# Performance work log

Measured on AMD Instinct MI355X. Metric: run time of the kernel, lower is better.

Reference implementation:

```python
import jax, jax.numpy as jnp
import numpy as np

NUM_HEADS = 4
IN_CHANNELS = 256
SCALE = IN_CHANNELS ** (-0.5)  # scaled=True uses in_channels, not hidden


def setup_inputs() -> dict:
    key = jax.random.key(0)
    ks = jax.random.split(key, 6)
    B, C, H, W = 8, 256, 48, 48
    hid = 128
    std_e = (2.0 / (3 * hid)) ** 0.5   # kaiming fan_out for 1x1 conv
    std_o = (2.0 / C) ** 0.5
    return {
        "x0": jax.random.normal(ks[0], (B, C, H, W), jnp.float32),
        "x1": jax.random.normal(ks[1], (B, C, H, W), jnp.float32),
        "embed_w0": jax.random.normal(ks[2], (3 * hid, C), jnp.float32) * std_e,
        "embed_b0": jnp.zeros((3 * hid,), jnp.float32),
        "embed_w1": jax.random.normal(ks[3], (3 * hid, C), jnp.float32) * std_e,
        "embed_b1": jnp.zeros((3 * hid,), jnp.float32),
        "out_w0": jax.random.normal(ks[4], (hid * NUM_HEADS, C), jnp.float32) * std_o,
        "out_b0": jnp.zeros((C,), jnp.float32),
        "out_w1": jax.random.normal(ks[5], (hid * NUM_HEADS, C), jnp.float32) * std_o,
        "out_b1": jnp.zeros((C,), jnp.float32),
    }


def _embed(x, w, b):
    # 1x1 conv: [B,C,H,W] x [3h,C] -> [B,3h,H,W], then flatten spatial and split q/k/v
    e = jnp.einsum('bchw,oc->bohw', x, w) + b[None, :, None, None]
    B, O, H, W = e.shape
    e = e.reshape(B, O, H * W)
    return jnp.split(e, 3, axis=1)  # each [B, h, N]


def _attend(q, k, v):
    # q from the OTHER stream; softmax over keys (last dim)
    attn = jax.nn.softmax(jnp.einsum('bcm,bcn->bmn', q, k) * SCALE, axis=-1)
    return jnp.einsum('bmn,bcn->bcm', attn, v)  # [B, h, N]


def _output(h, x, w, b):
    # all NUM_HEADS heads are identical (same embed conv reused per head),
    # so the concat along channels is a tile of one head.
    hh = jnp.tile(h, (1, NUM_HEADS, 1))  # [B, h*nh, N]
    # 1x1 transposed conv == pointwise linear with weight [h*nh, C]
    o = jnp.einsum('bcm,co->bom', hh, w) + b[None, :, None]
    return o.reshape(x.shape) + x  # residual


def reference(x0, x1, embed_w0, embed_b0, embed_w1, embed_b1,
              out_w0, out_b0, out_w1, out_b1):
    q0, k0, v0 = _embed(x0, embed_w0, embed_b0)
    q1, k1, v1 = _embed(x1, embed_w1, embed_b1)
    h0 = _attend(q1, k0, v0)  # stream 0 queried by stream 1's q
    h1 = _attend(q0, k1, v1)
    out0 = _output(h0, x0, out_w0, out_b0)
    out1 = _output(h1, x1, out_w1, out_b1)
    return (out0, out1)
```

## Files before the change

kernel.cpp:

```cpp
#include <hip/hip_runtime.h>
#include <stdint.h>

#define B_   8
#define C_   256
#define N_   2304
#define HID  128
#define O3   384
#define NH   4
#define SCALE 0.0625f
#define QPRE 0.09016844f

typedef unsigned short u16;
typedef short  bf8  __attribute__((ext_vector_type(8)));
typedef float  f4   __attribute__((ext_vector_type(4)));
typedef u16    u16x8 __attribute__((ext_vector_type(8)));

#define MFMA(a,b,c) __builtin_amdgcn_mfma_f32_16x16x32_bf16((a),(b),(c),0,0,0)

static __device__ __forceinline__ u16 f2bf(float f){
    union { float f; unsigned int i; } v; v.f = f;
    unsigned int r = v.i + 0x7FFFu + ((v.i >> 16) & 1u);
    return (u16)(r >> 16);
}
static __device__ __forceinline__ float fexp2(float x){
#if __has_builtin(__builtin_amdgcn_exp2f)
    return __builtin_amdgcn_exp2f(x);
#else
    return __expf(x * 0.69314718f);
#endif
}
static __device__ __forceinline__ u16 hi16(float f){
    union { float f; unsigned int i; } v; v.f = f;
    return (u16)(v.i >> 16);
}
static __device__ __forceinline__ void dma16(const void* g, void* l){
    __builtin_amdgcn_global_load_lds(
        (const __attribute__((address_space(1))) void*)g,
        (__attribute__((address_space(3))) void*)l, 16, 0, 0);
}

__global__ __launch_bounds__(256) void k_prep(const float* __restrict__ ew0,
                                              const float* __restrict__ ew1,
                                              const float* __restrict__ ow0,
                                              const float* __restrict__ ow1,
                                              u16* __restrict__ Wbf,
                                              u16* __restrict__ weff){
    int bid = blockIdx.x;
    if (bid < 192){
        int s = bid >= 96 ? 1 : 0;
        int xb = bid - s*96;
        const float* w = s ? ew1 : ew0;
        u16* o = Wbf + (size_t)s * (O3 * C_);
        int idx = (xb * 256 + threadIdx.x) * 4;
        float4 v = *reinterpret_cast<const float4*>(&w[idx]);
        o[idx+0] = f2bf(v.x); o[idx+1] = f2bf(v.y);
        o[idx+2] = f2bf(v.z); o[idx+3] = f2bf(v.w);
    } else {
        int gid = (bid - 192) * 256 + threadIdx.x;
        int oc = gid & 255, hc = (gid >> 8) & 127, s = gid >> 15;
        const float* w = s ? ow1 : ow0;
        float acc = 0.f;
        #pragma unroll
        for (int h = 0; h < NH; ++h) acc += w[(h*HID + hc)*C_ + oc];
        weff[(s*C_ + oc)*HID + hc] = f2bf(acc);
    }
}

__global__ __launch_bounds__(256, 3) void k_embed_fused(
        const float* __restrict__ x0, const float* __restrict__ x1,
        const u16* __restrict__ Wbf,
        const float* __restrict__ b0, const float* __restrict__ b1,
        u16* __restrict__ Qc, u16* __restrict__ Kc, u16* __restrict__ Vc){
    __shared__ __align__(16) u16 Xs[64*272];
    __shared__ __align__(16) u16 tile[64*72];
    int z = blockIdx.y, bb = z >> 1, s = z & 1;
    const float* X = (s ? x1 : x0) + (size_t)bb * (C_ * N_);
    const u16* W = Wbf + (size_t)s * (O3 * C_);
    const float* bias = s ? b1 : b0;
    int n0 = blockIdx.x * 64;
    int t = threadIdx.x;
    int lane = t & 63, wave = t >> 6;
    int l16 = lane & 15, quad = lane >> 4;

    {
        int lr = t >> 4, lc = (t & 15) * 4;
        int row = t >> 3, col8 = (t & 7) * 8;
        for (int cb = 0; cb < 4; ++cb){
            int c0 = cb * 64;
            #pragma unroll
            for (int rep = 0; rep < 4; ++rep){
                int c = lr + rep * 16;
                float4 v = *reinterpret_cast<const float4*>(
                    &X[(size_t)(c0 + c) * N_ + n0 + lc]);
                tile[c*65 + lc+0] = f2bf(v.x); tile[c*65 + lc+1] = f2bf(v.y);
                tile[c*65 + lc+2] = f2bf(v.z); tile[c*65 + lc+3] = f2bf(v.w);
            }
            __syncthreads();
            #pragma unroll
            for (int rep = 0; rep < 2; ++rep){
                int n = row + rep * 32;
                u16x8 v;
                #pragma unroll
                for (int j = 0; j < 8; ++j) v[j] = tile[(col8 + j)*65 + n];
                *reinterpret_cast<u16x8*>(&Xs[n*272 + c0 + col8]) = v;
            }
            __syncthreads();
        }
    }

    size_t zq = (size_t)z * (N_ * HID);
    int ncw = n0 >> 6;
    for (int og = 0; og < 6; ++og){
        int o0 = og*64 + wave*16;
        f4 acc[4] = {f4{0,0,0,0}, f4{0,0,0,0}, f4{0,0,0,0}, f4{0,0,0,0}};
        #pragma unroll
        for (int kk = 0; kk < 8; ++kk){
            bf8 a = *reinterpret_cast<const bf8*>(&W[(o0 + l16)*C_ + kk*32 + quad*8]);
            #pragma unroll
            for (int nt = 0; nt < 4; ++nt){
                bf8 bv = *reinterpret_cast<const bf8*>(
                    &Xs[(nt*16 + l16)*272 + kk*32 + quad*8]);
                acc[nt] = MFMA(a, bv, acc[nt]);
            }
        }
        float4 bv4 = *reinterpret_cast<const float4*>(&bias[o0 + quad*4]);
        float bb4[4] = {bv4.x, bv4.y, bv4.z, bv4.w};
        #pragma unroll
        for (int nt = 0; nt < 4; ++nt)
            #pragma unroll
            for (int r = 0; r < 4; ++r){
                float e = acc[nt][r] + bb4[r];
                if (og < 2) e *= QPRE;
                tile[(wave*16 + quad*4 + r)*72 + nt*16 + l16] = f2bf(e);
            }
        __syncthreads();
        #pragma unroll
        for (int rep = 0; rep < 2; ++rep){
            int idx = t + rep*256;
            if (og < 2){
                int n = idx & 63, g8 = idx >> 6;
                u16x8 v;
                #pragma unroll
                for (int j = 0; j < 8; ++j) v[j] = tile[(g8*8 + j)*72 + n];
                int ng = n0 + n;
                *reinterpret_cast<u16x8*>(&Qc[zq + (size_t)(ng>>4)*2048
                        + (og*8 + g8)*128 + (ng & 15)*8]) = v;
            } else if (og < 4){
                int n = idx & 63, cc = idx >> 6;
                u16x8 v;
                #pragma unroll
                for (int j = 0; j < 8; ++j) v[j] = tile[(cc*8 + j)*72 + n];
                *reinterpret_cast<u16x8*>(&Kc[zq
                        + (size_t)(ncw*16 + (og-2)*8 + cc)*512 + n*8]) = v;
            } else {
                int hl = idx & 63, p = idx >> 6;
                u16x8 v = *reinterpret_cast<const u16x8*>(&tile[hl*72 + p*8]);
                *reinterpret_cast<u16x8*>(&Vc[zq + (size_t)(ncw*8 + p)*1024
                        + ((og-4)*64 + hl)*8]) = v;
            }
        }
        __syncthreads();
    }
}

__global__ __launch_bounds__(256, 3) void k_attn_out(const u16* __restrict__ Qt,
        const u16* __restrict__ Kc, const u16* __restrict__ Vc,
        const u16* __restrict__ weff,
        const float* __restrict__ ob0, const float* __restrict__ ob1,
        const float* __restrict__ x0, const float* __restrict__ x1,
        float* __restrict__ out){
    __shared__ __align__(16) u16 kbuf[64*128];
    __shared__ __align__(16) u16 vbuf[64*128];
    __shared__ __align__(16) u16 smem[8*16*72];
    int bx = blockIdx.x;
    int xcd = bx & 7, t = bx >> 3;
    int z  = xcd*2 + (t >= 36 ? 1 : 0);
    int mt = (t >= 36) ? (t - 36) : t;
    int b = z >> 1, s = z & 1;
    const u16* Q = Qt + (size_t)(b*2 + (1 - s)) * (N_ * HID);
    const u16* K = Kc + (size_t)(b*2 + s)       * (N_ * HID);
    const u16* V = Vc + (size_t)(b*2 + s)       * (N_ * HID);
    const u16* Wf   = weff + (size_t)s * (C_ * HID);
    const float* bias = s ? ob1 : ob0;
    const float* X = (s ? x1 : x0) + (size_t)b * (C_ * N_);
    float* O = out + (size_t)s * ((size_t)B_ * C_ * N_) + (size_t)b * (C_ * N_);
    int lane = threadIdx.x & 63, wave = threadIdx.x >> 6;
    int l16 = lane & 15, quad = lane >> 4;
    int m0 = mt * 64 + wave * 16;

    bf8 aq[4];
    {
        const u16* Qb = Q + (size_t)(m0 >> 4)*2048 + l16*8;
        #pragma unroll
        for (int kk = 0; kk < 4; ++kk)
            aq[kk] = *reinterpret_cast<const bf8*>(&Qb[(kk*4 + quad)*128]);
    }

    bf8 ones;
    #pragma unroll
    for (int j = 0; j < 8; ++j) ones[j] = (short)0x3F80;

    f4 oacc[8];
    #pragma unroll
    for (int ct = 0; ct < 8; ++ct) oacc[ct] = f4{0,0,0,0};
    f4 sumacc = f4{0,0,0,0};

    const char* Kb = (const char*)K;
    const char* Vb = (const char*)V;

    for (int nc = 0; nc < N_/64; ++nc){
        __syncthreads();
        #pragma unroll
        for (int j = 0; j < 4; ++j){
            int ik = wave*4 + j;
            dma16(Kb + ((size_t)(nc*16 + ik)*512 + lane*8)*2, &kbuf[ik*512]);
        }
        #pragma unroll
        for (int j = 0; j < 4; ++j){
            int iv = wave*4 + j;
            dma16(Vb + ((size_t)(nc*8 + (iv>>1))*1024 + (iv&1)*512 + lane*8)*2,
                  &vbuf[iv*512]);
        }
        __syncthreads();
        f4 sacc[4] = {f4{0,0,0,0}, f4{0,0,0,0}, f4{0,0,0,0}, f4{0,0,0,0}};
        #pragma unroll
        for (int kk = 0; kk < 4; ++kk)
            #pragma unroll
            for (int nt = 0; nt < 4; ++nt){
                bf8 bk = *reinterpret_cast<const bf8*>(&kbuf[((kk*4+quad)*64 + nt*16 + l16)*8]);
                sacc[nt] = MFMA(aq[kk], bk, sacc[nt]);
            }
        u16* pw = smem + (wave*2 + (nc & 1)) * (16*72);
        #pragma unroll
        for (int nt = 0; nt < 4; ++nt)
            #pragma unroll
            for (int r = 0; r < 4; ++r)
                pw[(quad*4 + r)*72 + nt*16 + l16] = hi16(fexp2(sacc[nt][r]));
        #pragma unroll
        for (int kk2 = 0; kk2 < 2; ++kk2){
            bf8 ap = *reinterpret_cast<const bf8*>(&pw[l16*72 + kk2*32 + quad*8]);
            sumacc = MFMA(ap, ones, sumacc);
            #pragma unroll
            for (int ct = 0; ct < 8; ++ct){
                bf8 bv = *reinterpret_cast<const bf8*>(&vbuf[((kk2*4+quad)*128 + ct*16 + l16)*8]);
                oacc[ct] = MFMA(ap, bv, oacc[ct]);
            }
        }
    }

    __syncthreads();
    float inv[4];
    #pragma unroll
    for (int r = 0; r < 4; ++r) inv[r] = 1.0f / sumacc[r];
    #pragma unroll
    for (int ct = 0; ct < 8; ++ct)
        #pragma unroll
        for (int r = 0; r < 4; ++r)
            smem[(wave*16 + quad*4 + r)*136 + ct*16 + l16] = f2bf(oacc[ct][r] * inv[r]);
    __syncthreads();

    int mb = mt * 64;
    int oc0 = wave * 64;
    f4 acc2[4][4];
    #pragma unroll
    for (int ot = 0; ot < 4; ++ot)
        #pragma unroll
        for (int nt = 0; nt < 4; ++nt) acc2[ot][nt] = f4{0,0,0,0};
    #pragma unroll
    for (int kk = 0; kk < 4; ++kk){
        bf8 bh[4];
        #pragma unroll
        for (int nt = 0; nt < 4; ++nt)
            bh[nt] = *reinterpret_cast<const bf8*>(&smem[(nt*16 + l16)*136 + kk*32 + quad*8]);
        #pragma unroll
        for (int ot = 0; ot < 4; ++ot){
            bf8 a = *reinterpret_cast<const bf8*>(&Wf[(oc0 + ot*16 + l16)*HID + kk*32 + quad*8]);
            #pragma unroll
            for (int nt = 0; nt < 4; ++nt)
                acc2[ot][nt] = MFMA(a, bh[nt], acc2[ot][nt]);
        }
    }
    #pragma unroll
    for (int ot = 0; ot < 4; ++ot)
        #pragma unroll
        for (int nt = 0; nt < 4; ++nt){
            int m = mb + nt*16 + l16;
            #pragma unroll
            for (int r = 0; r < 4; ++r){
                int oc = oc0 + ot*16 + quad*4 + r;
                O[(size_t)oc*N_ + m] = acc2[ot][nt][r] + bias[oc] + X[(size_t)oc*N_ + m];
            }
        }
}

extern "C" void kernel_launch(void* const* d_in, const int* in_sizes, int n_in,
                              void* d_out, int out_size, void* d_ws, size_t ws_size,
                              hipStream_t stream){
    const float* x0  = (const float*)d_in[0];
    const float* x1  = (const float*)d_in[1];
    const float* ew0 = (const float*)d_in[2];
    const float* eb0 = (const float*)d_in[3];
    const float* ew1 = (const float*)d_in[4];
    const float* eb1 = (const float*)d_in[5];
    const float* ow0 = (const float*)d_in[6];
    const float* ob0 = (const float*)d_in[7];
    const float* ow1 = (const float*)d_in[8];
    const float* ob1 = (const float*)d_in[9];

    u16* ws = (u16*)d_ws;
    const size_t QT_E = (size_t)16 * N_ * HID;
    u16* Qc   = ws;
    u16* Kc   = Qc + QT_E;
    u16* Vc   = Kc + QT_E;
    u16* Wbf  = Vc + QT_E;
    u16* weff = Wbf + (size_t)2 * O3 * C_;

    k_prep       <<<dim3(448),    dim3(256), 0, stream>>>(ew0, ew1, ow0, ow1, Wbf, weff);
    k_embed_fused<<<dim3(36, 16), dim3(256), 0, stream>>>(x0, x1, Wbf, eb0, eb1, Qc, Kc, Vc);
    k_attn_out   <<<dim3(576),    dim3(256), 0, stream>>>(Qc, Kc, Vc, weff, ob0, ob1,
                                                          x0, x1, (float*)d_out);
}
```

Baseline: 211.5 us.

## Fold weight prep into embed kernel and halve embed column tile

Removes the separate k_prep launch. The embed kernel now converts fp32 embed weights to bf16 on the fly and an extra grid row computes the head-summed output weights. The spatial tile shrinks from 64 to 32 columns, doubling the embed grid and raising occupancy to 4 blocks per CU with smaller LDS. The cost is redundant weight loads and conversion in every block, plus less weight reuse per block.

```diff
diff --git a/kernel.cpp b/kernel.cpp
--- a/kernel.cpp
+++ b/kernel.cpp
@@ -14,6 +14,7 @@
 typedef short  bf8  __attribute__((ext_vector_type(8)));
 typedef float  f4   __attribute__((ext_vector_type(4)));
 typedef u16    u16x8 __attribute__((ext_vector_type(8)));
+typedef u16    u16x4 __attribute__((ext_vector_type(4)));
 
 #define MFMA(a,b,c) __builtin_amdgcn_mfma_f32_16x16x32_bf16((a),(b),(c),0,0,0)
 
@@ -39,125 +40,128 @@
         (__attribute__((address_space(3))) void*)l, 16, 0, 0);
 }
 
-__global__ __launch_bounds__(256) void k_prep(const float* __restrict__ ew0,
-                                              const float* __restrict__ ew1,
-                                              const float* __restrict__ ow0,
-                                              const float* __restrict__ ow1,
-                                              u16* __restrict__ Wbf,
-                                              u16* __restrict__ weff){
-    int bid = blockIdx.x;
-    if (bid < 192){
-        int s = bid >= 96 ? 1 : 0;
-        int xb = bid - s*96;
-        const float* w = s ? ew1 : ew0;
-        u16* o = Wbf + (size_t)s * (O3 * C_);
-        int idx = (xb * 256 + threadIdx.x) * 4;
-        float4 v = *reinterpret_cast<const float4*>(&w[idx]);
-        o[idx+0] = f2bf(v.x); o[idx+1] = f2bf(v.y);
-        o[idx+2] = f2bf(v.z); o[idx+3] = f2bf(v.w);
-    } else {
-        int gid = (bid - 192) * 256 + threadIdx.x;
-        int oc = gid & 255, hc = (gid >> 8) & 127, s = gid >> 15;
+__global__ __launch_bounds__(256, 4) void k_embed_fused(
+        const float* __restrict__ x0, const float* __restrict__ x1,
+        const float* __restrict__ ew0, const float* __restrict__ ew1,
+        const float* __restrict__ ow0, const float* __restrict__ ow1,
+        const float* __restrict__ b0, const float* __restrict__ b1,
+        u16* __restrict__ Qc, u16* __restrict__ Kc, u16* __restrict__ Vc,
+        u16* __restrict__ weff){
+    __shared__ __align__(16) u16 tmp[256*36];
+    __shared__ __align__(16) u16 Xs[32*280];
+    int t = threadIdx.x;
+
+    if (blockIdx.y == 16){
+        int bx = blockIdx.x;
+        if (bx >= 64) return;
+        int gid = bx*256 + t;
+        int s = gid >> 13, oc = (gid >> 5) & 255, hc0 = (gid & 31) * 4;
         const float* w = s ? ow1 : ow0;
-        float acc = 0.f;
-        #pragma unroll
-        for (int h = 0; h < NH; ++h) acc += w[(h*HID + hc)*C_ + oc];
-        weff[(s*C_ + oc)*HID + hc] = f2bf(acc);
-    }
-}
-
-__global__ __launch_bounds__(256, 3) void k_embed_fused(
-        const float* __restrict__ x0, const float* __restrict__ x1,
-        const u16* __restrict__ Wbf,
-        const float* __restrict__ b0, const float* __restrict__ b1,
-        u16* __restrict__ Qc, u16* __restrict__ Kc, u16* __restrict__ Vc){
-    __shared__ __align__(16) u16 Xs[64*272];
-    __shared__ __align__(16) u16 tile[64*72];
+        u16x4 v;
+        #pragma unroll
+        for (int i = 0; i < 4; ++i){
+            float acc = 0.f;
+            #pragma unroll
+            for (int h = 0; h < NH; ++h) acc += w[(h*HID + hc0 + i)*C_ + oc];
+            v[i] = f2bf(acc);
+        }
+        *reinterpret_cast<u16x4*>(&weff[(s*C_ + oc)*HID + hc0]) = v;
+        return;
+    }
+
     int z = blockIdx.y, bb = z >> 1, s = z & 1;
-    const float* X = (s ? x1 : x0) + (size_t)bb * (C_ * N_);
-    const u16* W = Wbf + (size_t)s * (O3 * C_);
+    const float* X    = (s ? x1 : x0) + (size_t)bb * (C_ * N_);
+    const float* Wf32 = s ? ew1 : ew0;
     const float* bias = s ? b1 : b0;
-    int n0 = blockIdx.x * 64;
-    int t = threadIdx.x;
+    int n0 = blockIdx.x * 32;
     int lane = t & 63, wave = t >> 6;
     int l16 = lane & 15, quad = lane >> 4;
 
     {
-        int lr = t >> 4, lc = (t & 15) * 4;
-        int row = t >> 3, col8 = (t & 7) * 8;
-        for (int cb = 0; cb < 4; ++cb){
-            int c0 = cb * 64;
-            #pragma unroll
-            for (int rep = 0; rep < 4; ++rep){
-                int c = lr + rep * 16;
-                float4 v = *reinterpret_cast<const float4*>(
-                    &X[(size_t)(c0 + c) * N_ + n0 + lc]);
-                tile[c*65 + lc+0] = f2bf(v.x); tile[c*65 + lc+1] = f2bf(v.y);
-                tile[c*65 + lc+2] = f2bf(v.z); tile[c*65 + lc+3] = f2bf(v.w);
-            }
-            __syncthreads();
-            #pragma unroll
-            for (int rep = 0; rep < 2; ++rep){
-                int n = row + rep * 32;
-                u16x8 v;
-                #pragma unroll
-                for (int j = 0; j < 8; ++j) v[j] = tile[(col8 + j)*65 + n];
-                *reinterpret_cast<u16x8*>(&Xs[n*272 + c0 + col8]) = v;
-            }
-            __syncthreads();
-        }
-    }
+        int cbase = t >> 3, cq = t & 7;
+        float4 xr[8];
+        #pragma unroll
+        for (int rep = 0; rep < 8; ++rep)
+            xr[rep] = *reinterpret_cast<const float4*>(
+                &X[(size_t)(cbase + rep*32) * N_ + n0 + cq*4]);
+        #pragma unroll
+        for (int rep = 0; rep < 8; ++rep){
+            int c = cbase + rep*32;
+            u16x4 v;
+            v[0] = f2bf(xr[rep].x); v[1] = f2bf(xr[rep].y);
+            v[2] = f2bf(xr[rep].z); v[3] = f2bf(xr[rep].w);
+            *reinterpret_cast<u16x4*>(&tmp[c*36 + cq*4]) = v;
+        }
+    }
+    __syncthreads();
+    {
+        int n = t & 31, c8b = t >> 5;
+        #pragma unroll
+        for (int rep = 0; rep < 4; ++rep){
+            int c8 = c8b + rep*8;
+            u16x8 v;
+            #pragma unroll
+            for (int j = 0; j < 8; ++j) v[j] = tmp[(c8*8 + j)*36 + n];
+            *reinterpret_cast<u16x8*>(&Xs[n*280 + c8*8]) = v;
+        }
+    }
+    __syncthreads();
 
     size_t zq = (size_t)z * (N_ * HID);
-    int ncw = n0 >> 6;
+    int ncw = blockIdx.x >> 1;
+    u16* Es = tmp;
     for (int og = 0; og < 6; ++og){
         int o0 = og*64 + wave*16;
-        f4 acc[4] = {f4{0,0,0,0}, f4{0,0,0,0}, f4{0,0,0,0}, f4{0,0,0,0}};
+        f4 acc[2] = {f4{0,0,0,0}, f4{0,0,0,0}};
         #pragma unroll
         for (int kk = 0; kk < 8; ++kk){
-            bf8 a = *reinterpret_cast<const bf8*>(&W[(o0 + l16)*C_ + kk*32 + quad*8]);
-            #pragma unroll
-            for (int nt = 0; nt < 4; ++nt){
+            const float* wp = &Wf32[(size_t)(o0 + l16)*C_ + kk*32 + quad*8];
+            float4 wa = *reinterpret_cast<const float4*>(wp);
+            float4 wb = *reinterpret_cast<const float4*>(wp + 4);
+            bf8 a;
+            a[0] = (short)f2bf(wa.x); a[1] = (short)f2bf(wa.y);
+            a[2] = (short)f2bf(wa.z); a[3] = (short)f2bf(wa.w);
+            a[4] = (short)f2bf(wb.x); a[5] = (short)f2bf(wb.y);
+            a[6] = (short)f2bf(wb.z); a[7] = (short)f2bf(wb.w);
+            #pragma unroll
+            for (int nt = 0; nt < 2; ++nt){
                 bf8 bv = *reinterpret_cast<const bf8*>(
-                    &Xs[(nt*16 + l16)*272 + kk*32 + quad*8]);
+                    &Xs[(nt*16 + l16)*280 + kk*32 + quad*8]);
                 acc[nt] = MFMA(a, bv, acc[nt]);
             }
         }
         float4 bv4 = *reinterpret_cast<const float4*>(&bias[o0 + quad*4]);
         float bb4[4] = {bv4.x, bv4.y, bv4.z, bv4.w};
         #pragma unroll
-        for (int nt = 0; nt < 4; ++nt)
+        for (int nt = 0; nt < 2; ++nt)
             #pragma unroll
             for (int r = 0; r < 4; ++r){
                 float e = acc[nt][r] + bb4[r];
                 if (og < 2) e *= QPRE;
-                tile[(wave*16 + quad*4 + r)*72 + nt*16 + l16] = f2bf(e);
+                Es[(wave*16 + quad*4 + r)*40 + nt*16 + l16] = f2bf(e);
             }
         __syncthreads();
-        #pragma unroll
-        for (int rep = 0; rep < 2; ++rep){
-            int idx = t + rep*256;
-            if (og < 2){
-                int n = idx & 63, g8 = idx >> 6;
-                u16x8 v;
-                #pragma unroll
-                for (int j = 0; j < 8; ++j) v[j] = tile[(g8*8 + j)*72 + n];
-                int ng = n0 + n;
-                *reinterpret_cast<u16x8*>(&Qc[zq + (size_t)(ng>>4)*2048
-                        + (og*8 + g8)*128 + (ng & 15)*8]) = v;
-            } else if (og < 4){
-                int n = idx & 63, cc = idx >> 6;
-                u16x8 v;
-                #pragma unroll
-                for (int j = 0; j < 8; ++j) v[j] = tile[(cc*8 + j)*72 + n];
-                *reinterpret_cast<u16x8*>(&Kc[zq
-                        + (size_t)(ncw*16 + (og-2)*8 + cc)*512 + n*8]) = v;
-            } else {
-                int hl = idx & 63, p = idx >> 6;
-                u16x8 v = *reinterpret_cast<const u16x8*>(&tile[hl*72 + p*8]);
-                *reinterpret_cast<u16x8*>(&Vc[zq + (size_t)(ncw*8 + p)*1024
-                        + ((og-4)*64 + hl)*8]) = v;
-            }
+        if (og < 2){
+            int n = t & 31, g8 = t >> 5;
+            u16x8 v;
+            #pragma unroll
+            for (int j = 0; j < 8; ++j) v[j] = Es[(g8*8 + j)*40 + n];
+            int ng = n0 + n;
+            *reinterpret_cast<u16x8*>(&Qc[zq + (size_t)(ng>>4)*2048
+                    + (og*8 + g8)*128 + (ng & 15)*8]) = v;
+        } else if (og < 4){
+            int n = t & 31, cc = t >> 5;
+            u16x8 v;
+            #pragma unroll
+            for (int j = 0; j < 8; ++j) v[j] = Es[(cc*8 + j)*40 + n];
+            *reinterpret_cast<u16x8*>(&Kc[zq + (size_t)(ncw*16 + (og-2)*8 + cc)*512
+                    + ((n0 + n) & 63)*8]) = v;
+        } else {
+            int hl = t & 63, pp = t >> 6;
+            u16x8 v = *reinterpret_cast<const u16x8*>(&Es[hl*40 + pp*8]);
+            int p = ((n0 + pp*8) >> 3) & 7;
+            *reinterpret_cast<u16x8*>(&Vc[zq + (size_t)(ncw*8 + p)*1024
+                    + ((og-4)*64 + hl)*8]) = v;
         }
         __syncthreads();
     }
@@ -312,11 +316,10 @@
     u16* Qc   = ws;
     u16* Kc   = Qc + QT_E;
     u16* Vc   = Kc + QT_E;
-    u16* Wbf  = Vc + QT_E;
-    u16* weff = Wbf + (size_t)2 * O3 * C_;
-
-    k_prep       <<<dim3(448),    dim3(256), 0, stream>>>(ew0, ew1, ow0, ow1, Wbf, weff);
-    k_embed_fused<<<dim3(36, 16), dim3(256), 0, stream>>>(x0, x1, Wbf, eb0, eb1, Qc, Kc, Vc);
-    k_attn_out   <<<dim3(576),    dim3(256), 0, stream>>>(Qc, Kc, Vc, weff, ob0, ob1,
-                                                          x0, x1, (float*)d_out);
-}
+    u16* weff = Vc + QT_E;
+
+    k_embed_fused<<<dim3(72, 17), dim3(256), 0, stream>>>(
+        x0, x1, ew0, ew1, ow0, ow1, eb0, eb1, Qc, Kc, Vc, weff);
+    k_attn_out   <<<dim3(576),    dim3(256), 0, stream>>>(
+        Qc, Kc, Vc, weff, ob0, ob1, x0, x1, (float*)d_out);
+}
```

Measured after the change: 243.6 us. 15.2% more time.

## Double-buffer K in LDS and prefetch V into registers in attention loop

Applied to the files above, without the earlier changes.

The attention loop now double-buffers the K tile in LDS. The next chunk's K is issued before the current chunk is computed, which removes one block barrier per iteration. V is no longer staged through LDS; each lane loads its V fragments straight from global memory into registers, one chunk ahead. s_setprio is also raised around the MFMA bursts. The aim is to hide global-load latency behind the matrix work, at the cost of 64 extra VGPRs, which may spill or lower occupancy under the 3-blocks launch bound.

```diff
diff --git a/kernel.cpp b/kernel.cpp
--- a/kernel.cpp
+++ b/kernel.cpp
@@ -169,8 +169,7 @@
         const float* __restrict__ ob0, const float* __restrict__ ob1,
         const float* __restrict__ x0, const float* __restrict__ x1,
         float* __restrict__ out){
-    __shared__ __align__(16) u16 kbuf[64*128];
-    __shared__ __align__(16) u16 vbuf[64*128];
+    __shared__ __align__(16) u16 kbuf[2][64*128];
     __shared__ __align__(16) u16 smem[8*16*72];
     int bx = blockIdx.x;
     int xcd = bx & 7, t = bx >> 3;
@@ -206,49 +205,69 @@
     f4 sumacc = f4{0,0,0,0};
 
     const char* Kb = (const char*)K;
-    const char* Vb = (const char*)V;
+    const u16* vq = V + quad*1024 + l16*8;
+
+#define STAGE_K(nc_, bsel_) do {                                             \
+        _Pragma("unroll")                                                    \
+        for (int j = 0; j < 4; ++j){                                         \
+            int ik = wave*4 + j;                                             \
+            dma16(Kb + ((size_t)((nc_)*16 + ik)*512 + lane*8)*2,             \
+                  &kbuf[bsel_][ik*512]);                                     \
+        }                                                                    \
+    } while(0)
+
+    STAGE_K(0, 0);
+    bf8 vf[16];
+    #pragma unroll
+    for (int kk2 = 0; kk2 < 2; ++kk2)
+        #pragma unroll
+        for (int ct = 0; ct < 8; ++ct)
+            vf[kk2*8 + ct] = *reinterpret_cast<const bf8*>(&vq[kk2*4096 + ct*128]);
 
     for (int nc = 0; nc < N_/64; ++nc){
+        int cur = nc & 1;
         __syncthreads();
-        #pragma unroll
-        for (int j = 0; j < 4; ++j){
-            int ik = wave*4 + j;
-            dma16(Kb + ((size_t)(nc*16 + ik)*512 + lane*8)*2, &kbuf[ik*512]);
-        }
-        #pragma unroll
-        for (int j = 0; j < 4; ++j){
-            int iv = wave*4 + j;
-            dma16(Vb + ((size_t)(nc*8 + (iv>>1))*1024 + (iv&1)*512 + lane*8)*2,
-                  &vbuf[iv*512]);
-        }
-        __syncthreads();
+        if (nc + 1 < N_/64) STAGE_K(nc + 1, cur ^ 1);
+        const u16* kb = kbuf[cur];
         f4 sacc[4] = {f4{0,0,0,0}, f4{0,0,0,0}, f4{0,0,0,0}, f4{0,0,0,0}};
+        __builtin_amdgcn_s_setprio(1);
         #pragma unroll
         for (int kk = 0; kk < 4; ++kk)
             #pragma unroll
             for (int nt = 0; nt < 4; ++nt){
-                bf8 bk = *reinterpret_cast<const bf8*>(&kbuf[((kk*4+quad)*64 + nt*16 + l16)*8]);
+                bf8 bk = *reinterpret_cast<const bf8*>(
+                    &kb[((kk*4 + quad)*64 + nt*16 + l16)*8]);
                 sacc[nt] = MFMA(aq[kk], bk, sacc[nt]);
             }
-        u16* pw = smem + (wave*2 + (nc & 1)) * (16*72);
+        __builtin_amdgcn_s_setprio(0);
+        u16* pw = smem + (wave*2 + cur) * (16*72);
         #pragma unroll
         for (int nt = 0; nt < 4; ++nt)
             #pragma unroll
             for (int r = 0; r < 4; ++r)
                 pw[(quad*4 + r)*72 + nt*16 + l16] = hi16(fexp2(sacc[nt][r]));
+        size_t vnext = (size_t)(nc + 1) * 8192;
         #pragma unroll
         for (int kk2 = 0; kk2 < 2; ++kk2){
             bf8 ap = *reinterpret_cast<const bf8*>(&pw[l16*72 + kk2*32 + quad*8]);
+            __builtin_amdgcn_s_setprio(1);
             sumacc = MFMA(ap, ones, sumacc);
             #pragma unroll
-            for (int ct = 0; ct < 8; ++ct){
-                bf8 bv = *reinterpret_cast<const bf8*>(&vbuf[((kk2*4+quad)*128 + ct*16 + l16)*8]);
-                oacc[ct] = MFMA(ap, bv, oacc[ct]);
-            }
-        }
-    }
+            for (int ct = 0; ct < 8; ++ct)
+                oacc[ct] = MFMA(ap, vf[kk2*8 + ct], oacc[ct]);
+            __builtin_amdgcn_s_setprio(0);
+            if (nc + 1 < N_/64){
+                #pragma unroll
+                for (int ct = 0; ct < 8; ++ct)
+                    vf[kk2*8 + ct] = *reinterpret_cast<const bf8*>(
+                        &vq[vnext + kk2*4096 + ct*128]);
+            }
+        }
+    }
+#undef STAGE_K
 
     __syncthreads();
+    u16* Hm = smem;
     float inv[4];
     #pragma unroll
     for (int r = 0; r < 4; ++r) inv[r] = 1.0f / sumacc[r];
@@ -256,7 +275,7 @@
     for (int ct = 0; ct < 8; ++ct)
         #pragma unroll
         for (int r = 0; r < 4; ++r)
-            smem[(wave*16 + quad*4 + r)*136 + ct*16 + l16] = f2bf(oacc[ct][r] * inv[r]);
+            Hm[(wave*16 + quad*4 + r)*136 + ct*16 + l16] = f2bf(oacc[ct][r] * inv[r]);
     __syncthreads();
 
     int mb = mt * 64;
@@ -271,7 +290,7 @@
         bf8 bh[4];
         #pragma unroll
         for (int nt = 0; nt < 4; ++nt)
-            bh[nt] = *reinterpret_cast<const bf8*>(&smem[(nt*16 + l16)*136 + kk*32 + quad*8]);
+            bh[nt] = *reinterpret_cast<const bf8*>(&Hm[(nt*16 + l16)*136 + kk*32 + quad*8]);
         #pragma unroll
         for (int ot = 0; ot < 4; ++ot){
             bf8 a = *reinterpret_cast<const bf8*>(&Wf[(oc0 + ot*16 + l16)*HID + kk*32 + quad*8]);
```

Result: slower. 217.2 us (+2.7%).
